# Performance work log

Measured on AMD Instinct MI355X. Metric: run time of the kernel, lower is better.

The kernel has to match this reference:

```python
import jax, jax.numpy as jnp
import numpy as np

T, B, E, H = 256, 8, 512, 32
EXP = 512            # number of expanded (periodic-image) keys
SMOOTH = 20.0        # smooth_factor


def setup_inputs() -> dict:
    key = jax.random.key(0)
    ks = jax.random.split(key, 12)
    s = 1.0 / np.sqrt(E)
    return {
        "query": jax.random.normal(ks[0], (T, B, E), dtype=jnp.float32),
        "outcell_index": jax.random.randint(ks[1], (B, EXP), 0, T),
        "expand_mask": jax.random.bernoulli(ks[2], 0.1, (B, EXP)),
        "key_padding_mask": jax.random.bernoulli(ks[3], 0.1, (B, T)),
        "local_attention_weight": jax.random.uniform(ks[4], (B, T, T + EXP), dtype=jnp.float32),
        "Wq": jax.random.normal(ks[5], (E, E), dtype=jnp.float32) * s,
        "bq": jnp.zeros((E,), dtype=jnp.float32),
        "Wk": jax.random.normal(ks[6], (E, E), dtype=jnp.float32) * s,   # k_bias=False
        "Wv": jax.random.normal(ks[7], (E, E), dtype=jnp.float32) * s,
        "bv": jnp.zeros((E,), dtype=jnp.float32),
        "Wo": jax.random.normal(ks[8], (E, E), dtype=jnp.float32) * s,
        "bo": jnp.zeros((E,), dtype=jnp.float32),
    }


def reference(query, outcell_index, expand_mask, key_padding_mask,
              local_attention_weight, Wq, bq, Wk, Wv, bv, Wo, bo):
    t, b, e = query.shape
    hd = e // H
    # QKV projections (torch Linear: y = x @ W.T + b)
    q = jnp.einsum('tbe,fe->tbf', query, Wq) + bq
    k = jnp.einsum('tbe,fe->tbf', query, Wk)          # no k bias
    v = jnp.einsum('tbe,fe->tbf', query, Wv) + bv
    # PBC gather-expand K/V along the time axis
    oc = outcell_index.T[:, :, None]                  # [EXP, B, 1]
    k = jnp.concatenate([k, jnp.take_along_axis(k, oc, axis=0)], axis=0)  # [S,B,E]
    v = jnp.concatenate([v, jnp.take_along_axis(v, oc, axis=0)], axis=0)
    s_len = k.shape[0]
    # [len, B, E] -> [B, H, len, hd]
    qh = q.reshape(t, b, H, hd).transpose(1, 2, 0, 3)
    kh = k.reshape(s_len, b, H, hd).transpose(1, 2, 0, 3)
    vh = v.reshape(s_len, b, H, hd).transpose(1, 2, 0, 3)
    # NOTE: forward() never applies self.scaling in this path (faithful)
    scores = jnp.einsum('bhtd,bhsd->bhts', qh, kh)    # [B,H,T,S]
    law = local_attention_weight[:, None]             # [B,1,T,S]
    scores = (scores + SMOOTH) * law - SMOOTH         # smooth softmax
    kpm = jnp.concatenate([key_padding_mask, expand_mask], axis=1)  # [B,S]
    scores = jnp.where(kpm[:, None, None, :], -jnp.inf, scores)
    probs = jax.nn.softmax(scores, axis=-1)
    probs = probs * law                               # post-softmax reweight
    attn = jnp.einsum('bhts,bhsd->bhtd', probs, vh)   # [B,H,T,hd]
    attn = attn.transpose(2, 0, 1, 3).reshape(t, b, e)
    return jnp.einsum('tbe,fe->tbf', attn, Wo) + bo
```

## Files before the change

kernel.cpp:

```cpp
#include <hip/hip_runtime.h>
#include <stdint.h>

#define T_ 256
#define B_ 8
#define E_ 512
#define H_ 32
#define HD_ 16
#define EXP_ 512
#define S_ 768
#define M_ 2048
#define SMOOTH_ 20.0f
#define PSTR 40
#define VSTR 800
#define OSTR 20
#define LOG2E_ 1.44269504f
#define MB0_  (-100.988655f)

typedef __attribute__((ext_vector_type(8)))  short bf16x8;
typedef __attribute__((ext_vector_type(4)))  float f32x4;
typedef __attribute__((ext_vector_type(16))) float f32x16;

__device__ __forceinline__ unsigned int pku(float a, float b)
{
    return ((__float_as_uint(a) + 0x8000u) >> 16) |
           ((__float_as_uint(b) + 0x8000u) & 0xFFFF0000u);
}
__device__ __forceinline__ ushort bf1(float a)
{
    unsigned int u = __float_as_uint(a);
    u = u + 0x7FFFu + ((u >> 16) & 1u);
    return (ushort)(u >> 16);
}

union U16 { uint4 u; bf16x8 v; };

__global__ __launch_bounds__(1024, 4)
void qkv_attn_kernel(const float* __restrict__ X,
                     const float* __restrict__ Wq, const float* __restrict__ Wk,
                     const float* __restrict__ Wv,
                     const float* __restrict__ bq, const float* __restrict__ bv,
                     const float* __restrict__ LAW,
                     const int* __restrict__ kpm, const int* __restrict__ em,
                     const int* __restrict__ oc, ushort* __restrict__ Ab)
{
    __shared__ __align__(16) char raw[102400];
    ushort* Ks  = (ushort*)(raw);
    ushort* Vt  = (ushort*)(raw + 24576);
    ushort* Qi  = (ushort*)(raw + 50176);
    float*  msf = (float*) (raw + 58368);
    ushort* Pbb = (ushort*)(raw + 61440);
    ushort* As  = (ushort*)(raw);
    ushort* Bs  = (ushort*)(raw + 36864);
    float*  Obuf= (float*) (raw);
    float*  Zb  = (float*) (raw + 58368);
    ushort* Ob  = Qi;

    const int bh  = blockIdx.x;
    const int b   = bh & 7;
    const int h   = bh >> 3;
    const int tid = threadIdx.x;
    const int w   = tid >> 6;
    const int l   = tid & 63;

    const int r0 = tid >> 3;
    const int c8 = tid & 7;
    const float* Xc0 = &X[((size_t)r0 * 8 + b) * E_ + c8 * 8];
    const float* Xc1 = Xc0 + (size_t)128 * 8 * E_;

    const int wr = tid >> 3;
    const bool wload = (tid < 384);
    const float* Wsel = (wr < 16) ? Wq : (wr < 32 ? Wk : Wv);
    const float* Wr = &Wsel[((size_t)(h * 16 + (wr & 15))) * E_ + c8 * 8];
    ushort* Bxw = &Bs[wr * 72 + c8 * 8];

    f32x4 acc[3];
#pragma unroll
    for (int m = 0; m < 3; ++m) acc[m] = (f32x4){0.f, 0.f, 0.f, 0.f};

    float4 xa0, xa1, xb0, xb1, wp0, wp1;
    xa0 = *(const float4*)&Xc0[0]; xa1 = *(const float4*)&Xc0[4];
    xb0 = *(const float4*)&Xc1[0]; xb1 = *(const float4*)&Xc1[4];
    if (wload) { wp0 = *(const float4*)&Wr[0]; wp1 = *(const float4*)&Wr[4]; }

    const int ln = l & 15;
    const int lg = l >> 4;

    for (int it = 0; it < 8; ++it) {
        __syncthreads();
        *(uint4*)&As[r0 * 72 + c8 * 8] =
            make_uint4(pku(xa0.x, xa0.y), pku(xa0.z, xa0.w),
                       pku(xa1.x, xa1.y), pku(xa1.z, xa1.w));
        *(uint4*)&As[(r0 + 128) * 72 + c8 * 8] =
            make_uint4(pku(xb0.x, xb0.y), pku(xb0.z, xb0.w),
                       pku(xb1.x, xb1.y), pku(xb1.z, xb1.w));
        if (wload)
            *(uint4*)&Bxw[0] = make_uint4(pku(wp0.x, wp0.y), pku(wp0.z, wp0.w),
                                          pku(wp1.x, wp1.y), pku(wp1.z, wp1.w));
        __syncthreads();
        if (it < 7) {
            Xc0 += 64; Xc1 += 64;
            xa0 = *(const float4*)&Xc0[0]; xa1 = *(const float4*)&Xc0[4];
            xb0 = *(const float4*)&Xc1[0]; xb1 = *(const float4*)&Xc1[4];
            if (wload) { Wr += 64; wp0 = *(const float4*)&Wr[0]; wp1 = *(const float4*)&Wr[4]; }
        }
#pragma unroll
        for (int kb = 0; kb < 2; ++kb) {
            bf16x8 af = *(const bf16x8*)&As[(w * 16 + ln) * 72 + kb * 32 + lg * 8];
#pragma unroll
            for (int m = 0; m < 3; ++m) {
                bf16x8 bfm = *(const bf16x8*)&Bs[(m * 16 + ln) * 72 + kb * 32 + lg * 8];
                acc[m] = __builtin_amdgcn_mfma_f32_16x16x32_bf16(af, bfm, acc[m], 0, 0, 0);
            }
        }
    }

    __syncthreads();

    {
        const float bqv = bq[h * 16 + ln];
        const float bvv = bv[h * 16 + ln];
#pragma unroll
        for (int r = 0; r < 4; ++r) {
            const int t = w * 16 + lg * 4 + r;
            Qi[t * 16 + ln]   = bf1(acc[0][r] + bqv);
            Ks[t * 16 + ln]   = bf1(acc[1][r]);
            Vt[ln * VSTR + t] = bf1(acc[2][r] + bvv);
        }
    }
    __syncthreads();

    if (tid < 512) {
        const int j   = tid;
        const int src = oc[b * EXP_ + j];
        uint4 k0 = *(const uint4*)&Ks[src * 16];
        uint4 k1 = *(const uint4*)&Ks[src * 16 + 8];
        *(uint4*)&Ks[(T_ + j) * 16]     = k0;
        *(uint4*)&Ks[(T_ + j) * 16 + 8] = k1;
    } else {
        const int j   = tid - 512;
        const int src = oc[b * EXP_ + j];
#pragma unroll
        for (int d = 0; d < 16; ++d)
            Vt[d * VSTR + T_ + j] = Vt[d * VSTR + src];
    }
    if (tid < 768) {
        const int s = tid;
        const int m = (s < T_) ? kpm[b * T_ + s] : em[b * EXP_ + (s - T_)];
        msf[s] = m ? -1.0e5f : MB0_;
    }
    __syncthreads();

    const int slane = l & 31;
    const int khalf = l >> 5;
    const int tl = l & 15;
    const int kg = l >> 4;
    const int tq = w & 7;
    const int sh = w >> 3;

    bf16x8 qf = *(const bf16x8*)&Qi[(tq * 32 + slane) * 16 + khalf * 8];

    const f32x16 zero16 = {0.f,0.f,0.f,0.f,0.f,0.f,0.f,0.f,
                           0.f,0.f,0.f,0.f,0.f,0.f,0.f,0.f};
    f32x4 o0 = {0.f, 0.f, 0.f, 0.f};
    f32x4 o1 = {0.f, 0.f, 0.f, 0.f};
    float zacc[16];
#pragma unroll
    for (int r = 0; r < 16; ++r) zacc[r] = 0.f;

    const float* lawb = &LAW[((size_t)b * T_ + tq * 32 + khalf * 4) * S_ + slane];
    ushort* pw = &Pbb[w * 32 * PSTR + slane];
    ushort* pt = &Pbb[w * 32 * PSTR];

    for (int i = sh * 12; i < sh * 12 + 12; ++i) {
        bf16x8 kf = *(const bf16x8*)&Ks[(i * 32 + slane) * 16 + khalf * 8];

        float lw[16];
        const float* lp = lawb + i * 32;
#pragma unroll
        for (int r = 0; r < 16; ++r)
            lw[r] = lp[(size_t)((r & 3) + 8 * (r >> 2)) * S_];

        f32x16 sc = __builtin_amdgcn_mfma_f32_32x32x16_bf16(qf, kf, zero16, 0, 0, 0);
        const float mb = msf[i * 32 + slane];

#pragma unroll
        for (int r = 0; r < 16; ++r) {
            const float lwK = lw[r] * LOG2E_;
            const float arg = __builtin_fmaf(sc[r], lwK,
                              __builtin_fmaf(lwK, SMOOTH_, mb));
            const float e = __builtin_amdgcn_exp2f(arg);
            zacc[r] += e;
            const float p = e * lw[r];
            pw[((r & 3) + 8 * (r >> 2) + 4 * khalf) * PSTR] =
                (ushort)((__float_as_uint(p) + 0x8000u) >> 16);
        }

        bf16x8 vf = *(const bf16x8*)&Vt[tl * VSTR + i * 32 + kg * 8];
        {
            const ushort* pr0 = &pt[(0 * 16 + tl) * PSTR + kg * 8];
            U16 u;
            uint2 a0 = *(const uint2*)pr0;
            uint2 a1 = *(const uint2*)(pr0 + 4);
            u.u = make_uint4(a0.x, a0.y, a1.x, a1.y);
            o0 = __builtin_amdgcn_mfma_f32_16x16x32_bf16(vf, u.v, o0, 0, 0, 0);
            const ushort* pr1 = &pt[(1 * 16 + tl) * PSTR + kg * 8];
            uint2 b0 = *(const uint2*)pr1;
            uint2 b1 = *(const uint2*)(pr1 + 4);
            u.u = make_uint4(b0.x, b0.y, b1.x, b1.y);
            o1 = __builtin_amdgcn_mfma_f32_16x16x32_bf16(vf, u.v, o1, 0, 0, 0);
        }
    }

#pragma unroll
    for (int m = 1; m < 32; m <<= 1) {
#pragma unroll
        for (int r = 0; r < 16; ++r)
            zacc[r] += __shfl_xor(zacc[r], m);
    }

    __syncthreads();

    if (l == 0 || l == 32) {
#pragma unroll
        for (int r = 0; r < 16; ++r)
            Zb[sh * 256 + tq * 32 + (r & 3) + 8 * (r >> 2) + 4 * khalf] = zacc[r];
    }
    if (sh == 1) {
#pragma unroll
        for (int th = 0; th < 2; ++th) {
            const f32x4 o = th ? o1 : o0;
            *(float4*)&Obuf[((size_t)(tq * 32 + th * 16 + tl)) * OSTR + kg * 4] =
                make_float4(o[0], o[1], o[2], o[3]);
        }
    }
    __syncthreads();

    if (sh == 0) {
#pragma unroll
        for (int th = 0; th < 2; ++th) {
            const int t = tq * 32 + th * 16 + tl;
            const float Zt  = Zb[t] + Zb[256 + t];
            const float inv = (Zt > 0.f) ? 1.f / Zt : 0.f;
            float4 po = *(const float4*)&Obuf[(size_t)t * OSTR + kg * 4];
            const f32x4 o = th ? o1 : o0;
            float ov[4] = {(o[0] + po.x) * inv, (o[1] + po.y) * inv,
                           (o[2] + po.z) * inv, (o[3] + po.w) * inv};
            *(uint*)&Ob[t * 16 + kg * 4]     = pku(ov[0], ov[1]);
            *(uint*)&Ob[t * 16 + kg * 4 + 2] = pku(ov[2], ov[3]);
        }
    }
    __syncthreads();

    {
        const int t  = tid >> 2;
        const int q4 = tid & 3;
        *(uint2*)&Ab[((size_t)(t * 8 + b)) * E_ + h * 16 + q4 * 4] =
            *(const uint2*)&Ob[t * 16 + q4 * 4];
    }
}

__global__ __launch_bounds__(256, 2)
void out_gemm(const ushort* __restrict__ Ab, const float* __restrict__ Wo,
              const float* __restrict__ bo, float* __restrict__ dst)
{
    __shared__ __align__(16) ushort sbuf[96 * 136];
    ushort* As = sbuf;
    ushort* Bs = sbuf + 32 * 136;

    const int n0 = blockIdx.x * 64;
    const int m0 = blockIdx.y * 32;

    const int tid = threadIdx.x;
    const int arow = tid >> 3;
    const int acol = (tid & 7) * 16;
    const int brow = tid >> 2;
    const int bcol = (tid & 3) * 32;

    const ushort* Ap = &Ab[(size_t)(m0 + arow) * E_ + acol];
    const float*  Wp = &Wo[(size_t)(n0 + brow) * E_ + bcol];

    f32x4 acc[2];
    acc[0] = (f32x4){0.f, 0.f, 0.f, 0.f};
    acc[1] = (f32x4){0.f, 0.f, 0.f, 0.f};

    uint4  ha0 = *(const uint4*)&Ap[0];
    uint4  ha1 = *(const uint4*)&Ap[8];
    float4 f0 = *(const float4*)&Wp[0];
    float4 f1 = *(const float4*)&Wp[4];
    float4 f2 = *(const float4*)&Wp[8];
    float4 f3 = *(const float4*)&Wp[12];
    float4 f4 = *(const float4*)&Wp[16];
    float4 f5 = *(const float4*)&Wp[20];
    float4 f6 = *(const float4*)&Wp[24];
    float4 f7 = *(const float4*)&Wp[28];

    const int l  = tid & 63;
    const int w  = tid >> 6;
    const int wm = w & 1;
    const int wn = w >> 1;
    const int lq = l >> 4;
    const int ln = l & 15;

    for (int it = 0; it < 4; ++it) {
        __syncthreads();
        *(uint4*)&As[arow * 136 + acol]     = ha0;
        *(uint4*)&As[arow * 136 + acol + 8] = ha1;
        *(uint4*)&Bs[brow * 136 + bcol]      = make_uint4(pku(f0.x, f0.y), pku(f0.z, f0.w),
                                                          pku(f1.x, f1.y), pku(f1.z, f1.w));
        *(uint4*)&Bs[brow * 136 + bcol + 8]  = make_uint4(pku(f2.x, f2.y), pku(f2.z, f2.w),
                                                          pku(f3.x, f3.y), pku(f3.z, f3.w));
        *(uint4*)&Bs[brow * 136 + bcol + 16] = make_uint4(pku(f4.x, f4.y), pku(f4.z, f4.w),
                                                          pku(f5.x, f5.y), pku(f5.z, f5.w));
        *(uint4*)&Bs[brow * 136 + bcol + 24] = make_uint4(pku(f6.x, f6.y), pku(f6.z, f6.w),
                                                          pku(f7.x, f7.y), pku(f7.z, f7.w));
        __syncthreads();
        if (it < 3) {
            Ap += 128; Wp += 128;
            ha0 = *(const uint4*)&Ap[0];
            ha1 = *(const uint4*)&Ap[8];
            f0 = *(const float4*)&Wp[0];
            f1 = *(const float4*)&Wp[4];
            f2 = *(const float4*)&Wp[8];
            f3 = *(const float4*)&Wp[12];
            f4 = *(const float4*)&Wp[16];
            f5 = *(const float4*)&Wp[20];
            f6 = *(const float4*)&Wp[24];
            f7 = *(const float4*)&Wp[28];
        }
#pragma unroll
        for (int kb = 0; kb < 4; ++kb) {
            bf16x8 af  = *(const bf16x8*)&As[(wm * 16 + ln) * 136 + kb * 32 + lq * 8];
            bf16x8 bv0 = *(const bf16x8*)&Bs[(wn * 32 + ln) * 136 + kb * 32 + lq * 8];
            bf16x8 bv1 = *(const bf16x8*)&Bs[(wn * 32 + 16 + ln) * 136 + kb * 32 + lq * 8];
            acc[0] = __builtin_amdgcn_mfma_f32_16x16x32_bf16(af, bv0, acc[0], 0, 0, 0);
            acc[1] = __builtin_amdgcn_mfma_f32_16x16x32_bf16(af, bv1, acc[1], 0, 0, 0);
        }
    }

    const float bo0 = bo[n0 + wn * 32 + ln];
    const float bo1 = bo[n0 + wn * 32 + 16 + ln];

    __syncthreads();
    float* Lf = (float*)sbuf;
#pragma unroll
    for (int j = 0; j < 2; ++j) {
        const float bb = j ? bo1 : bo0;
        const f32x4 a = acc[j];
#pragma unroll
        for (int r = 0; r < 4; ++r)
            Lf[(wm * 16 + lq * 4 + r) * 68 + wn * 32 + j * 16 + ln] = a[r] + bb;
    }
    __syncthreads();

    {
        const int orow = tid >> 3;
        const int oc8  = (tid & 7) * 8;
        float* dp = &dst[(size_t)(m0 + orow) * E_ + n0 + oc8];
        float4 v0 = *(const float4*)&Lf[orow * 68 + oc8];
        float4 v1 = *(const float4*)&Lf[orow * 68 + oc8 + 4];
        *(float4*)&dp[0] = v0;
        *(float4*)&dp[4] = v1;
    }
}

extern "C" void kernel_launch(void* const* d_in, const int* in_sizes, int n_in,
                              void* d_out, int out_size, void* d_ws, size_t ws_size,
                              hipStream_t stream)
{
    const float* query = (const float*)d_in[0];
    const int*   oc    = (const int*)d_in[1];
    const int*   em    = (const int*)d_in[2];
    const int*   kpm   = (const int*)d_in[3];
    const float* law   = (const float*)d_in[4];
    const float* Wq    = (const float*)d_in[5];
    const float* bq    = (const float*)d_in[6];
    const float* Wk    = (const float*)d_in[7];
    const float* Wv    = (const float*)d_in[8];
    const float* bv    = (const float*)d_in[9];
    const float* Wo    = (const float*)d_in[10];
    const float* bo    = (const float*)d_in[11];
    float* out = (float*)d_out;

    ushort* Ab = (ushort*)d_ws;

    qkv_attn_kernel<<<B_ * H_, 1024, 0, stream>>>(query, Wq, Wk, Wv, bq, bv,
                                                  law, kpm, em, oc, Ab);

    dim3 go(E_ / 64, M_ / 32, 1);
    out_gemm<<<go, 256, 0, stream>>>(Ab, Wo, bo, out);
}
```

Measured before the change: 125.2 us.

## Stage LAW tiles through LDS with register prefetch and keep probabilities in registers

The score MFMA now runs with K and Q operands swapped, so each lane holds full score rows. Probabilities are packed to bf16 and exchanged across lane halves with permlane32_swap, then fed straight into a 32x32x16 PV MFMA, replacing the round trip through an LDS P buffer and the two 16x16 MFMAs. LAW tiles are loaded with coalesced float4 reads, double-buffered through registers one iteration ahead, and staged in a per-wave LDS area. The row sum now needs only one shuffle. The cost is more LDS (134 KB instead of 102 KB) and an epilogue where half the lanes sit idle, and the LDS writes for the next tile within a wave need correct ordering.

```diff
diff --git a/kernel.cpp b/kernel.cpp
--- a/kernel.cpp
+++ b/kernel.cpp
@@ -10,15 +10,16 @@
 #define S_ 768
 #define M_ 2048
 #define SMOOTH_ 20.0f
-#define PSTR 40
-#define VSTR 800
+#define VSTR 776
 #define OSTR 20
+#define LWSTR 36
 #define LOG2E_ 1.44269504f
 #define MB0_  (-100.988655f)
 
 typedef __attribute__((ext_vector_type(8)))  short bf16x8;
 typedef __attribute__((ext_vector_type(4)))  float f32x4;
 typedef __attribute__((ext_vector_type(16))) float f32x16;
+typedef __attribute__((ext_vector_type(2)))  unsigned int uint32x2;
 
 __device__ __forceinline__ unsigned int pku(float a, float b)
 {
@@ -43,16 +44,16 @@
                      const int* __restrict__ kpm, const int* __restrict__ em,
                      const int* __restrict__ oc, ushort* __restrict__ Ab)
 {
-    __shared__ __align__(16) char raw[102400];
+    __shared__ __align__(16) char raw[134400];
     ushort* Ks  = (ushort*)(raw);
     ushort* Vt  = (ushort*)(raw + 24576);
-    ushort* Qi  = (ushort*)(raw + 50176);
-    float*  msf = (float*) (raw + 58368);
-    ushort* Pbb = (ushort*)(raw + 61440);
+    ushort* Qi  = (ushort*)(raw + 49408);
+    float*  msf = (float*) (raw + 57600);
+    float*  LAWf= (float*) (raw + 60672);
     ushort* As  = (ushort*)(raw);
     ushort* Bs  = (ushort*)(raw + 36864);
     float*  Obuf= (float*) (raw);
-    float*  Zb  = (float*) (raw + 58368);
+    float*  Zb  = (float*) (raw + 57600);
     ushort* Ob  = Qi;
 
     const int bh  = blockIdx.x;
@@ -127,6 +128,29 @@
             Vt[ln * VSTR + t] = bf1(acc[2][r] + bvv);
         }
     }
+
+    const int tq = w & 7;
+    const int sh = w >> 3;
+    const int i0 = sh * 12;
+    const int iend = i0 + 12;
+    float* lws = &LAWf[w * 32 * LWSTR];
+    const int srow = l >> 1;
+    const int scol = (l & 1) * 16;
+    const float* gl = &LAW[((size_t)b * T_ + tq * 32 + srow) * S_ + scol];
+
+    float4 g0 = *(const float4*)&gl[i0 * 32 + 0];
+    float4 g1 = *(const float4*)&gl[i0 * 32 + 4];
+    float4 g2 = *(const float4*)&gl[i0 * 32 + 8];
+    float4 g3 = *(const float4*)&gl[i0 * 32 + 12];
+    *(float4*)&lws[srow * LWSTR + scol + 0]  = g0;
+    *(float4*)&lws[srow * LWSTR + scol + 4]  = g1;
+    *(float4*)&lws[srow * LWSTR + scol + 8]  = g2;
+    *(float4*)&lws[srow * LWSTR + scol + 12] = g3;
+    g0 = *(const float4*)&gl[(i0 + 1) * 32 + 0];
+    g1 = *(const float4*)&gl[(i0 + 1) * 32 + 4];
+    g2 = *(const float4*)&gl[(i0 + 1) * 32 + 8];
+    g3 = *(const float4*)&gl[(i0 + 1) * 32 + 12];
+
     __syncthreads();
 
     if (tid < 512) {
@@ -151,102 +175,91 @@
     __syncthreads();
 
     const int slane = l & 31;
-    const int khalf = l >> 5;
-    const int tl = l & 15;
-    const int kg = l >> 4;
-    const int tq = w & 7;
-    const int sh = w >> 3;
-
-    bf16x8 qf = *(const bf16x8*)&Qi[(tq * 32 + slane) * 16 + khalf * 8];
+    const int hi    = l >> 5;
+
+    bf16x8 qf = *(const bf16x8*)&Qi[(tq * 32 + slane) * 16 + hi * 8];
 
     const f32x16 zero16 = {0.f,0.f,0.f,0.f,0.f,0.f,0.f,0.f,
                            0.f,0.f,0.f,0.f,0.f,0.f,0.f,0.f};
-    f32x4 o0 = {0.f, 0.f, 0.f, 0.f};
-    f32x4 o1 = {0.f, 0.f, 0.f, 0.f};
-    float zacc[16];
-#pragma unroll
-    for (int r = 0; r < 16; ++r) zacc[r] = 0.f;
-
-    const float* lawb = &LAW[((size_t)b * T_ + tq * 32 + khalf * 4) * S_ + slane];
-    ushort* pw = &Pbb[w * 32 * PSTR + slane];
-    ushort* pt = &Pbb[w * 32 * PSTR];
-
-    for (int i = sh * 12; i < sh * 12 + 12; ++i) {
-        bf16x8 kf = *(const bf16x8*)&Ks[(i * 32 + slane) * 16 + khalf * 8];
-
-        float lw[16];
-        const float* lp = lawb + i * 32;
-#pragma unroll
-        for (int r = 0; r < 16; ++r)
-            lw[r] = lp[(size_t)((r & 3) + 8 * (r >> 2)) * S_];
-
-        f32x16 sc = __builtin_amdgcn_mfma_f32_32x32x16_bf16(qf, kf, zero16, 0, 0, 0);
-        const float mb = msf[i * 32 + slane];
-
+    f32x16 oacc = zero16;
+    float z = 0.f;
+
+    for (int i = i0; i < iend; ++i) {
+        bf16x8 kf = *(const bf16x8*)&Ks[(i * 32 + slane) * 16 + hi * 8];
+        f32x16 sc = __builtin_amdgcn_mfma_f32_32x32x16_bf16(kf, qf, zero16, 0, 0, 0);
+
+#pragma unroll
+        for (int ks = 0; ks < 2; ++ks) {
+            float pp[8];
+#pragma unroll
+            for (int gi = 0; gi < 2; ++gi) {
+                const int g = 2 * ks + gi;
+                const float4 lw4 = *(const float4*)&lws[slane * LWSTR + g * 8 + 4 * hi];
+                const float4 mb4 = *(const float4*)&msf[i * 32 + g * 8 + 4 * hi];
+                const float lwa[4] = {lw4.x, lw4.y, lw4.z, lw4.w};
+                const float mba[4] = {mb4.x, mb4.y, mb4.z, mb4.w};
+#pragma unroll
+                for (int c = 0; c < 4; ++c) {
+                    const float lwv = lwa[c];
+                    const float lwK = lwv * LOG2E_;
+                    const float arg = __builtin_fmaf(sc[8 * ks + 4 * gi + c], lwK,
+                                      __builtin_fmaf(lwK, SMOOTH_, mba[c]));
+                    const float e = __builtin_amdgcn_exp2f(arg);
+                    z += e;
+                    pp[4 * gi + c] = e * lwv;
+                }
+            }
+            const unsigned int cA0 = pku(pp[0], pp[1]);
+            const unsigned int cA2 = pku(pp[2], pp[3]);
+            const unsigned int cB0 = pku(pp[4], pp[5]);
+            const unsigned int cB2 = pku(pp[6], pp[7]);
+            uint32x2 s0 = __builtin_amdgcn_permlane32_swap(cA0, cB0, false, false);
+            uint32x2 s1 = __builtin_amdgcn_permlane32_swap(cA2, cB2, false, false);
+            U16 u;
+            u.u = make_uint4(s0.x, s1.x, s0.y, s1.y);
+            bf16x8 vf = *(const bf16x8*)&Vt[(l & 15) * VSTR + i * 32 + ks * 16 + hi * 8];
+            oacc = __builtin_amdgcn_mfma_f32_32x32x16_bf16(u.v, vf, oacc, 0, 0, 0);
+        }
+
+        if (i + 1 < iend) {
+            *(float4*)&lws[srow * LWSTR + scol + 0]  = g0;
+            *(float4*)&lws[srow * LWSTR + scol + 4]  = g1;
+            *(float4*)&lws[srow * LWSTR + scol + 8]  = g2;
+            *(float4*)&lws[srow * LWSTR + scol + 12] = g3;
+            if (i + 2 < iend) {
+                g0 = *(const float4*)&gl[(i + 2) * 32 + 0];
+                g1 = *(const float4*)&gl[(i + 2) * 32 + 4];
+                g2 = *(const float4*)&gl[(i + 2) * 32 + 8];
+                g3 = *(const float4*)&gl[(i + 2) * 32 + 12];
+            }
+        }
+    }
+
+    z += __shfl_xor(z, 32);
+
+    __syncthreads();
+
+    if (l < 32) Zb[sh * 256 + tq * 32 + l] = z;
+
+    const int dl = l & 15;
+    const bool dok = (l & 31) < 16;
+    if (sh == 1 && dok) {
 #pragma unroll
         for (int r = 0; r < 16; ++r) {
-            const float lwK = lw[r] * LOG2E_;
-            const float arg = __builtin_fmaf(sc[r], lwK,
-                              __builtin_fmaf(lwK, SMOOTH_, mb));
-            const float e = __builtin_amdgcn_exp2f(arg);
-            zacc[r] += e;
-            const float p = e * lw[r];
-            pw[((r & 3) + 8 * (r >> 2) + 4 * khalf) * PSTR] =
-                (ushort)((__float_as_uint(p) + 0x8000u) >> 16);
-        }
-
-        bf16x8 vf = *(const bf16x8*)&Vt[tl * VSTR + i * 32 + kg * 8];
-        {
-            const ushort* pr0 = &pt[(0 * 16 + tl) * PSTR + kg * 8];
-            U16 u;
-            uint2 a0 = *(const uint2*)pr0;
-            uint2 a1 = *(const uint2*)(pr0 + 4);
-            u.u = make_uint4(a0.x, a0.y, a1.x, a1.y);
-            o0 = __builtin_amdgcn_mfma_f32_16x16x32_bf16(vf, u.v, o0, 0, 0, 0);
-            const ushort* pr1 = &pt[(1 * 16 + tl) * PSTR + kg * 8];
-            uint2 b0 = *(const uint2*)pr1;
-            uint2 b1 = *(const uint2*)(pr1 + 4);
-            u.u = make_uint4(b0.x, b0.y, b1.x, b1.y);
-            o1 = __builtin_amdgcn_mfma_f32_16x16x32_bf16(vf, u.v, o1, 0, 0, 0);
-        }
-    }
-
-#pragma unroll
-    for (int m = 1; m < 32; m <<= 1) {
-#pragma unroll
-        for (int r = 0; r < 16; ++r)
-            zacc[r] += __shfl_xor(zacc[r], m);
-    }
-
-    __syncthreads();
-
-    if (l == 0 || l == 32) {
-#pragma unroll
-        for (int r = 0; r < 16; ++r)
-            Zb[sh * 256 + tq * 32 + (r & 3) + 8 * (r >> 2) + 4 * khalf] = zacc[r];
-    }
-    if (sh == 1) {
-#pragma unroll
-        for (int th = 0; th < 2; ++th) {
-            const f32x4 o = th ? o1 : o0;
-            *(float4*)&Obuf[((size_t)(tq * 32 + th * 16 + tl)) * OSTR + kg * 4] =
-                make_float4(o[0], o[1], o[2], o[3]);
-        }
-    }
-    __syncthreads();
-
-    if (sh == 0) {
-#pragma unroll
-        for (int th = 0; th < 2; ++th) {
-            const int t = tq * 32 + th * 16 + tl;
+            const int t = tq * 32 + (r & 3) + 8 * (r >> 2) + 4 * hi;
+            Obuf[t * OSTR + dl] = oacc[r];
+        }
+    }
+    __syncthreads();
+
+    if (sh == 0 && dok) {
+#pragma unroll
+        for (int r = 0; r < 16; ++r) {
+            const int t = tq * 32 + (r & 3) + 8 * (r >> 2) + 4 * hi;
             const float Zt  = Zb[t] + Zb[256 + t];
             const float inv = (Zt > 0.f) ? 1.f / Zt : 0.f;
-            float4 po = *(const float4*)&Obuf[(size_t)t * OSTR + kg * 4];
-            const f32x4 o = th ? o1 : o0;
-            float ov[4] = {(o[0] + po.x) * inv, (o[1] + po.y) * inv,
-                           (o[2] + po.z) * inv, (o[3] + po.w) * inv};
-            *(uint*)&Ob[t * 16 + kg * 4]     = pku(ov[0], ov[1]);
-            *(uint*)&Ob[t * 16 + kg * 4 + 2] = pku(ov[2], ov[3]);
+            const float ov  = (oacc[r] + Obuf[t * OSTR + dl]) * inv;
+            Ob[t * 16 + dl] = bf1(ov);
         }
     }
     __syncthreads();
```

Measured after the change: 125.3 us. About the same (+0.1%).

## Reuse output buffer for attention intermediate and restructure output GEMM per row-block

Applied to the files above, without the earlier changes.

The attention kernel now writes its bf16 result into the output buffer itself, with a row stride chosen so each row lines up with the matching fp32 output row. The output GEMM is rewritten so each 512-thread block owns 32 full rows. It loads those rows of A into LDS before overwriting them, then loops over all N tiles and streams Wo through LDS. Float-to-bf16 packing switches to the hardware v_cvt_pk_bf16_f32 instruction. The aim is to drop the workspace round trip and the extra conversion instructions, at the cost of far fewer GEMM blocks (64 instead of 512) and Wo being re-read by every block.

```diff
diff --git a/kernel.cpp b/kernel.cpp
--- a/kernel.cpp
+++ b/kernel.cpp
@@ -13,6 +13,7 @@
 #define PSTR 40
 #define VSTR 800
 #define OSTR 20
+#define ABST 1024
 #define LOG2E_ 1.44269504f
 #define MB0_  (-100.988655f)
 
@@ -24,6 +25,12 @@
 {
     return ((__float_as_uint(a) + 0x8000u) >> 16) |
            ((__float_as_uint(b) + 0x8000u) & 0xFFFF0000u);
+}
+__device__ __forceinline__ unsigned int cvtpk(float a, float b)
+{
+    unsigned int r;
+    asm("v_cvt_pk_bf16_f32 %0, %1, %2" : "=v"(r) : "v"(a), "v"(b));
+    return r;
 }
 __device__ __forceinline__ ushort bf1(float a)
 {
@@ -88,14 +95,14 @@
     for (int it = 0; it < 8; ++it) {
         __syncthreads();
         *(uint4*)&As[r0 * 72 + c8 * 8] =
-            make_uint4(pku(xa0.x, xa0.y), pku(xa0.z, xa0.w),
-                       pku(xa1.x, xa1.y), pku(xa1.z, xa1.w));
+            make_uint4(cvtpk(xa0.x, xa0.y), cvtpk(xa0.z, xa0.w),
+                       cvtpk(xa1.x, xa1.y), cvtpk(xa1.z, xa1.w));
         *(uint4*)&As[(r0 + 128) * 72 + c8 * 8] =
-            make_uint4(pku(xb0.x, xb0.y), pku(xb0.z, xb0.w),
-                       pku(xb1.x, xb1.y), pku(xb1.z, xb1.w));
+            make_uint4(cvtpk(xb0.x, xb0.y), cvtpk(xb0.z, xb0.w),
+                       cvtpk(xb1.x, xb1.y), cvtpk(xb1.z, xb1.w));
         if (wload)
-            *(uint4*)&Bxw[0] = make_uint4(pku(wp0.x, wp0.y), pku(wp0.z, wp0.w),
-                                          pku(wp1.x, wp1.y), pku(wp1.z, wp1.w));
+            *(uint4*)&Bxw[0] = make_uint4(cvtpk(wp0.x, wp0.y), cvtpk(wp0.z, wp0.w),
+                                          cvtpk(wp1.x, wp1.y), cvtpk(wp1.z, wp1.w));
         __syncthreads();
         if (it < 7) {
             Xc0 += 64; Xc1 += 64;
@@ -254,112 +261,95 @@
     {
         const int t  = tid >> 2;
         const int q4 = tid & 3;
-        *(uint2*)&Ab[((size_t)(t * 8 + b)) * E_ + h * 16 + q4 * 4] =
+        *(uint2*)&Ab[((size_t)(t * 8 + b)) * ABST + h * 16 + q4 * 4] =
             *(const uint2*)&Ob[t * 16 + q4 * 4];
     }
 }
 
-__global__ __launch_bounds__(256, 2)
-void out_gemm(const ushort* __restrict__ Ab, const float* __restrict__ Wo,
-              const float* __restrict__ bo, float* __restrict__ dst)
-{
-    __shared__ __align__(16) ushort sbuf[96 * 136];
-    ushort* As = sbuf;
-    ushort* Bs = sbuf + 32 * 136;
-
-    const int n0 = blockIdx.x * 64;
-    const int m0 = blockIdx.y * 32;
-
+__global__ __launch_bounds__(512, 2)
+void out_gemm(const float* __restrict__ Wo, const float* __restrict__ bo,
+              float* __restrict__ dst)
+{
+    __shared__ __align__(16) ushort As[32 * 520];
+    __shared__ __align__(16) ushort Bs[64 * 136];
+
+    const int m0  = blockIdx.x * 32;
     const int tid = threadIdx.x;
-    const int arow = tid >> 3;
-    const int acol = (tid & 7) * 16;
-    const int brow = tid >> 2;
-    const int bcol = (tid & 3) * 32;
-
-    const ushort* Ap = &Ab[(size_t)(m0 + arow) * E_ + acol];
-    const float*  Wp = &Wo[(size_t)(n0 + brow) * E_ + bcol];
-
-    f32x4 acc[2];
-    acc[0] = (f32x4){0.f, 0.f, 0.f, 0.f};
-    acc[1] = (f32x4){0.f, 0.f, 0.f, 0.f};
-
-    uint4  ha0 = *(const uint4*)&Ap[0];
-    uint4  ha1 = *(const uint4*)&Ap[8];
+    const int l   = tid & 63;
+    const int w   = tid >> 6;
+    const int wm  = w & 1;
+    const int wn  = w >> 1;
+    const int lq  = l >> 4;
+    const int ln  = l & 15;
+
+    {
+        const ushort* Abp = (const ushort*)dst;
+        const int r = tid >> 4;
+        const int c = (tid & 15) * 32;
+        const ushort* sp = &Abp[(size_t)(m0 + r) * ABST + c];
+        uint4 a0 = *(const uint4*)(sp);
+        uint4 a1 = *(const uint4*)(sp + 8);
+        uint4 a2 = *(const uint4*)(sp + 16);
+        uint4 a3 = *(const uint4*)(sp + 24);
+        ushort* dp = &As[r * 520 + c];
+        *(uint4*)(dp)      = a0;
+        *(uint4*)(dp + 8)  = a1;
+        *(uint4*)(dp + 16) = a2;
+        *(uint4*)(dp + 24) = a3;
+    }
+
+    float bov[8];
+#pragma unroll
+    for (int nt = 0; nt < 8; ++nt)
+        bov[nt] = bo[nt * 64 + wn * 16 + ln];
+
+    const int brow = tid >> 3;
+    const int bcol = (tid & 7) * 16;
+
+    const float* Wp = &Wo[(size_t)brow * E_ + bcol];
     float4 f0 = *(const float4*)&Wp[0];
     float4 f1 = *(const float4*)&Wp[4];
     float4 f2 = *(const float4*)&Wp[8];
     float4 f3 = *(const float4*)&Wp[12];
-    float4 f4 = *(const float4*)&Wp[16];
-    float4 f5 = *(const float4*)&Wp[20];
-    float4 f6 = *(const float4*)&Wp[24];
-    float4 f7 = *(const float4*)&Wp[28];
-
-    const int l  = tid & 63;
-    const int w  = tid >> 6;
-    const int wm = w & 1;
-    const int wn = w >> 1;
-    const int lq = l >> 4;
-    const int ln = l & 15;
-
-    for (int it = 0; it < 4; ++it) {
+
+    f32x4 acc = {0.f, 0.f, 0.f, 0.f};
+
+    for (int s = 0; s < 32; ++s) {
         __syncthreads();
-        *(uint4*)&As[arow * 136 + acol]     = ha0;
-        *(uint4*)&As[arow * 136 + acol + 8] = ha1;
-        *(uint4*)&Bs[brow * 136 + bcol]      = make_uint4(pku(f0.x, f0.y), pku(f0.z, f0.w),
-                                                          pku(f1.x, f1.y), pku(f1.z, f1.w));
-        *(uint4*)&Bs[brow * 136 + bcol + 8]  = make_uint4(pku(f2.x, f2.y), pku(f2.z, f2.w),
-                                                          pku(f3.x, f3.y), pku(f3.z, f3.w));
-        *(uint4*)&Bs[brow * 136 + bcol + 16] = make_uint4(pku(f4.x, f4.y), pku(f4.z, f4.w),
-                                                          pku(f5.x, f5.y), pku(f5.z, f5.w));
-        *(uint4*)&Bs[brow * 136 + bcol + 24] = make_uint4(pku(f6.x, f6.y), pku(f6.z, f6.w),
-                                                          pku(f7.x, f7.y), pku(f7.z, f7.w));
+        *(uint4*)&Bs[brow * 136 + bcol] =
+            make_uint4(cvtpk(f0.x, f0.y), cvtpk(f0.z, f0.w),
+                       cvtpk(f1.x, f1.y), cvtpk(f1.z, f1.w));
+        *(uint4*)&Bs[brow * 136 + bcol + 8] =
+            make_uint4(cvtpk(f2.x, f2.y), cvtpk(f2.z, f2.w),
+                       cvtpk(f3.x, f3.y), cvtpk(f3.z, f3.w));
         __syncthreads();
-        if (it < 3) {
-            Ap += 128; Wp += 128;
-            ha0 = *(const uint4*)&Ap[0];
-            ha1 = *(const uint4*)&Ap[8];
-            f0 = *(const float4*)&Wp[0];
-            f1 = *(const float4*)&Wp[4];
-            f2 = *(const float4*)&Wp[8];
-            f3 = *(const float4*)&Wp[12];
-            f4 = *(const float4*)&Wp[16];
-            f5 = *(const float4*)&Wp[20];
-            f6 = *(const float4*)&Wp[24];
-            f7 = *(const float4*)&Wp[28];
-        }
+        if (s < 31) {
+            const int sn = s + 1;
+            const float* Wn = &Wo[(size_t)((sn >> 2) * 64 + brow) * E_ +
+                                  (sn & 3) * 128 + bcol];
+            f0 = *(const float4*)&Wn[0];
+            f1 = *(const float4*)&Wn[4];
+            f2 = *(const float4*)&Wn[8];
+            f3 = *(const float4*)&Wn[12];
+        }
+        const int kt = s & 3;
 #pragma unroll
         for (int kb = 0; kb < 4; ++kb) {
-            bf16x8 af  = *(const bf16x8*)&As[(wm * 16 + ln) * 136 + kb * 32 + lq * 8];
-            bf16x8 bv0 = *(const bf16x8*)&Bs[(wn * 32 + ln) * 136 + kb * 32 + lq * 8];
-            bf16x8 bv1 = *(const bf16x8*)&Bs[(wn * 32 + 16 + ln) * 136 + kb * 32 + lq * 8];
-            acc[0] = __builtin_amdgcn_mfma_f32_16x16x32_bf16(af, bv0, acc[0], 0, 0, 0);
-            acc[1] = __builtin_amdgcn_mfma_f32_16x16x32_bf16(af, bv1, acc[1], 0, 0, 0);
-        }
-    }
-
-    const float bo0 = bo[n0 + wn * 32 + ln];
-    const float bo1 = bo[n0 + wn * 32 + 16 + ln];
-
-    __syncthreads();
-    float* Lf = (float*)sbuf;
-#pragma unroll
-    for (int j = 0; j < 2; ++j) {
-        const float bb = j ? bo1 : bo0;
-        const f32x4 a = acc[j];
-#pragma unroll
-        for (int r = 0; r < 4; ++r)
-            Lf[(wm * 16 + lq * 4 + r) * 68 + wn * 32 + j * 16 + ln] = a[r] + bb;
-    }
-    __syncthreads();
-
-    {
-        const int orow = tid >> 3;
-        const int oc8  = (tid & 7) * 8;
-        float* dp = &dst[(size_t)(m0 + orow) * E_ + n0 + oc8];
-        float4 v0 = *(const float4*)&Lf[orow * 68 + oc8];
-        float4 v1 = *(const float4*)&Lf[orow * 68 + oc8 + 4];
-        *(float4*)&dp[0] = v0;
-        *(float4*)&dp[4] = v1;
+            bf16x8 af = *(const bf16x8*)&As[(wm * 16 + ln) * 520 +
+                                            kt * 128 + kb * 32 + lq * 8];
+            bf16x8 bf = *(const bf16x8*)&Bs[(wn * 16 + ln) * 136 +
+                                            kb * 32 + lq * 8];
+            acc = __builtin_amdgcn_mfma_f32_16x16x32_bf16(af, bf, acc, 0, 0, 0);
+        }
+        if (kt == 3) {
+            const int nt = s >> 2;
+            const int gn = nt * 64 + wn * 16 + ln;
+            const float bb = bov[nt];
+#pragma unroll
+            for (int r = 0; r < 4; ++r)
+                dst[(size_t)(m0 + wm * 16 + lq * 4 + r) * E_ + gn] = acc[r] + bb;
+            acc = (f32x4){0.f, 0.f, 0.f, 0.f};
+        }
     }
 }
 
@@ -381,11 +371,11 @@
     const float* bo    = (const float*)d_in[11];
     float* out = (float*)d_out;
 
-    ushort* Ab = (ushort*)d_ws;
+    (void)d_ws; (void)ws_size;
+    ushort* Ab = (ushort*)d_out;
 
     qkv_attn_kernel<<<B_ * H_, 1024, 0, stream>>>(query, Wq, Wk, Wv, bq, bv,
                                                   law, kpm, em, oc, Ab);
 
-    dim3 go(E_ / 64, M_ / 32, 1);
-    out_gemm<<<go, 256, 0, stream>>>(Ab, Wo, bo, out);
-}
+    out_gemm<<<M_ / 32, 512, 0, stream>>>(Wo, bo, out);
+}
```

Measured after the change: 152.9 us. 1.22x slower.
